# Kernel tuning notes

Hardware: AMD Instinct MI355X
Metric: run time of the kernel (lower is better)

Reference implementation:

```python
import jax, jax.numpy as jnp
import numpy as np
import math

B, S, D_MODEL = 2, 2048, 1024
H = 16
DK = D_MODEL // H          # 64, down-proj per-stream dim
NOPE, ROPE = 128, 64
D_HEAD = NOPE + ROPE       # 192 = d_latent // H
D_LATENT = H * D_HEAD      # 3072
ROT_DIM = 2 * ((ROPE // 2) // 2)  # rotary dim actually rotated = qk_rope_dim//2 = 32
EPS = 1e-6


def _rmsnorm(x, w):
    out = x * jax.lax.rsqrt(jnp.mean(x * x, axis=-1, keepdims=True) + EPS)
    return out * w


def _apply_rope(x):
    # x: [b, h, s, d]; rotate first ROT_DIM channels, interleaved pairing
    s = x.shape[-2]
    inv_freq = 1.0 / (10000.0 ** (jnp.arange(0, ROT_DIM, 2, dtype=jnp.float32) / ROT_DIM))
    freqs = jnp.arange(s, dtype=jnp.float32)[:, None] * inv_freq[None, :]  # [s, ROT_DIM//2]
    freqs = jnp.repeat(freqs, 2, axis=-1)  # [s, ROT_DIM], (f0,f0,f1,f1,...)
    cos, sin = jnp.cos(freqs), jnp.sin(freqs)
    xl, xr = x[..., :ROT_DIM], x[..., ROT_DIM:]
    x1, x2 = xl[..., 0::2], xl[..., 1::2]
    rot = jnp.stack([-x2, x1], axis=-1).reshape(xl.shape)
    xl = xl * cos + rot * sin
    return jnp.concatenate([xl, xr], axis=-1)


def setup_inputs() -> dict:
    key = jax.random.key(0)
    ks = jax.random.split(key, 5)
    sc = 0.02
    x = jax.random.normal(ks[0], (B, S, D_MODEL), jnp.float32)
    mask = jnp.broadcast_to(jnp.tril(jnp.ones((S, S), jnp.int32)), (B, S, S))
    w_down = jax.random.normal(ks[1], (D_MODEL, 3 * DK), jnp.float32) * sc
    rms_w = jnp.ones((3 * DK,), jnp.float32)
    w_up = jax.random.normal(ks[2], (3 * DK, 3 * D_LATENT), jnp.float32) * sc
    w_o = jax.random.normal(ks[3], (D_LATENT, D_MODEL), jnp.float32) * sc
    return {"x": x, "mask": mask, "w_down": w_down, "rms_w": rms_w, "w_up": w_up, "w_o": w_o}


def reference(x, mask, w_down, rms_w, w_up, w_o):
    h = x @ w_down                        # [b, s, 3*dk]
    h = _rmsnorm(h, rms_w)
    qkv = h @ w_up                        # [b, s, 3*d_latent]
    q, k, v = jnp.split(qkv, 3, axis=-1)  # each [b, s, d_latent]

    def to_heads(t):
        # einops '(d h)': d outer, h inner
        return t.reshape(B, S, D_HEAD, H).transpose(0, 3, 1, 2)  # [b, h, s, d]

    q, k, v = to_heads(q), to_heads(k), to_heads(v)
    q_nope, q_rope = q[..., :NOPE], q[..., NOPE:]
    k_nope, k_rope = k[..., :NOPE], k[..., NOPE:]
    q_rope = _apply_rope(q_rope)
    k_rope = _apply_rope(k_rope)

    scores = (jnp.einsum('bhid,bhjd->bhij', q_nope, k_nope)
              + jnp.einsum('bhid,bhjd->bhij', q_rope, k_rope))
    scores = scores / math.sqrt(NOPE + ROPE)
    scores = jnp.where(mask[:, None] == 0, -1e9, scores)
    attn = jax.nn.softmax(scores, axis=-1)

    out = jnp.einsum('bhij,bhjd->bhid', attn, v)        # [b, h, s, d]
    out = out.transpose(0, 2, 1, 3).reshape(B, S, D_LATENT)  # 'b h s d -> b s (h d)'
    return out @ w_o
```

## Files before the change

### kernel.cpp

```cpp
#include <hip/hip_runtime.h>
#include <stdint.h>
#include <stddef.h>


typedef __bf16 bf16x8 __attribute__((ext_vector_type(8)));
typedef float  f32x4  __attribute__((ext_vector_type(4)));

#define MFMA16x16(a,b,c) __builtin_amdgcn_mfma_f32_16x16x32_bf16((a),(b),(c),0,0,0)

__device__ __forceinline__ uint16_t f2bf(float f){
  union { float f; uint32_t u; } v; v.f = f;
  uint32_t u = v.u + 0x7fffu + ((v.u >> 16) & 1u);
  return (uint16_t)(u >> 16);
}
__device__ __forceinline__ bf16x8 load_frag(const uint16_t* p){
  uint4 u = *reinterpret_cast<const uint4*>(p);
  return __builtin_bit_cast(bf16x8, u);
}
__device__ __forceinline__ f32x4 fzero(){
  f32x4 z = {0.f, 0.f, 0.f, 0.f};
  return z;
}
__device__ __forceinline__ uint32_t pack2(float a, float b){
  return (uint32_t)f2bf(a) | ((uint32_t)f2bf(b) << 16);
}
__device__ __forceinline__ void gl2lds16(const uint16_t* g, uint16_t* l){
  __builtin_amdgcn_global_load_lds(
      (const __attribute__((address_space(1))) uint32_t*)g,
      (__attribute__((address_space(3))) uint32_t*)l,
      16, 0, 0);
}

__global__ __launch_bounds__(256) void k_transpose_cvt(const float* __restrict__ in,
                                                       uint16_t* __restrict__ out,
                                                       int R, int C){
  __shared__ float t[32][33];
  const int tc = blockIdx.x * 32;
  const int tr = blockIdx.y * 32;
  const int j = threadIdx.x & 31, i0 = threadIdx.x >> 5;
  for(int ii = 0; ii < 4; ++ii){
    int r = i0 + ii * 8;
    t[r][j] = in[(size_t)(tr + r) * C + tc + j];
  }
  __syncthreads();
  for(int ii = 0; ii < 4; ++ii){
    int c = i0 + ii * 8;
    out[(size_t)(tc + c) * R + tr + j] = f2bf(t[j][c]);
  }
}

__global__ __launch_bounds__(256) void k_down_mfma(const float* __restrict__ x,
                                                   const uint16_t* __restrict__ wdt,
                                                   const float* __restrict__ rms_w,
                                                   uint16_t* __restrict__ h_out){
  __shared__ __align__(16) uint16_t as[32 * 64];
  __shared__ float hsq[32];
  const int tid  = threadIdx.x;
  const int wave = tid >> 6, lane = tid & 63;
  const int ml = lane & 15, qd = lane >> 4;
  const int m0 = blockIdx.x * 32;
  const int n0w = wave * 48;
  if(tid < 32) hsq[tid] = 0.f;

  f32x4 acc[2][3];
#pragma unroll
  for(int mt = 0; mt < 2; ++mt)
#pragma unroll
    for(int nt = 0; nt < 3; ++nt) acc[mt][nt] = fzero();

  const int srow = tid >> 3, sc = tid & 7;
  for(int kt = 0; kt < 16; ++kt){
    const float* src = x + (size_t)(m0 + srow) * 1024 + kt * 64 + sc * 8;
    float4 a = *reinterpret_cast<const float4*>(src);
    float4 b = *reinterpret_cast<const float4*>(src + 4);
    uint4 pk;
    pk.x = pack2(a.x, a.y); pk.y = pack2(a.z, a.w);
    pk.z = pack2(b.x, b.y); pk.w = pack2(b.z, b.w);
    __syncthreads();
    *reinterpret_cast<uint4*>(as + srow * 64 + ((sc ^ (srow & 7)) * 8)) = pk;
    __syncthreads();
#pragma unroll
    for(int kk = 0; kk < 2; ++kk){
      bf16x8 af[2];
#pragma unroll
      for(int mt = 0; mt < 2; ++mt){
        int row = mt * 16 + ml;
        af[mt] = load_frag(as + row * 64 + (((kk * 4 + qd) ^ (row & 7)) * 8));
      }
#pragma unroll
      for(int nt = 0; nt < 3; ++nt){
        bf16x8 bfr = load_frag(wdt + (size_t)(n0w + nt * 16 + ml) * 1024 + kt * 64 + kk * 32 + qd * 8);
#pragma unroll
        for(int mt = 0; mt < 2; ++mt)
          acc[mt][nt] = MFMA16x16(af[mt], bfr, acc[mt][nt]);
      }
    }
  }
  __syncthreads();
#pragma unroll
  for(int mt = 0; mt < 2; ++mt)
#pragma unroll
    for(int r = 0; r < 4; ++r){
      float s = acc[mt][0][r]*acc[mt][0][r] + acc[mt][1][r]*acc[mt][1][r] + acc[mt][2][r]*acc[mt][2][r];
#pragma unroll
      for(int off = 1; off < 16; off <<= 1) s += __shfl_xor(s, off);
      if(ml == 0) atomicAdd(&hsq[mt * 16 + qd * 4 + r], s);
    }
  __syncthreads();
  float rw[3];
#pragma unroll
  for(int nt = 0; nt < 3; ++nt) rw[nt] = rms_w[n0w + nt * 16 + ml];
#pragma unroll
  for(int mt = 0; mt < 2; ++mt)
#pragma unroll
    for(int r = 0; r < 4; ++r){
      int row = mt * 16 + qd * 4 + r;
      float scl = rsqrtf(hsq[row] * (1.0f / 192.0f) + 1e-6f);
#pragma unroll
      for(int nt = 0; nt < 3; ++nt)
        h_out[(size_t)(m0 + row) * 192 + n0w + nt * 16 + ml] = f2bf(acc[mt][nt][r] * scl * rw[nt]);
    }
}

__global__ __launch_bounds__(256) void k_gemm_up(const uint16_t* __restrict__ hmat,
                                                 const uint16_t* __restrict__ wt,
                                                 uint16_t* __restrict__ q_t,
                                                 uint16_t* __restrict__ k_t,
                                                 uint16_t* __restrict__ v_t){
  __shared__ __align__(16) uint16_t rp[16 * 129 * 8];
  const int wave = threadIdx.x >> 6, lane = threadIdx.x & 63;
  const int ml = lane & 15, qd = lane >> 4;
  const int m0 = blockIdx.y * 32;
  const int bx = blockIdx.x;
  const int which = bx / 6;
  const int d0b = (bx % 6) * 32;
  const int n0w = bx * 512 + wave * 128;
  const int d0w = d0b + wave * 8;

  bf16x8 af[2][6];
#pragma unroll
  for(int mt = 0; mt < 2; ++mt)
#pragma unroll
    for(int kk = 0; kk < 6; ++kk)
      af[mt][kk] = load_frag(hmat + (size_t)(m0 + mt * 16 + ml) * 192 + kk * 32 + qd * 8);

  f32x4 acc[8][2];
#pragma unroll
  for(int nt = 0; nt < 8; ++nt){ acc[nt][0] = fzero(); acc[nt][1] = fzero(); }
#pragma unroll
  for(int nt = 0; nt < 8; ++nt){
#pragma unroll
    for(int kk = 0; kk < 6; ++kk){
      bf16x8 b = load_frag(wt + (size_t)(n0w + nt * 16 + ml) * 192 + kk * 32 + qd * 8);
      acc[nt][0] = MFMA16x16(af[0][kk], b, acc[nt][0]);
      acc[nt][1] = MFMA16x16(af[1][kk], b, acc[nt][1]);
    }
  }

  const int b   = m0 >> 11;
  const int s0  = m0 & 2047;
  const int kt2 = s0 >> 6;
  const int row0 = s0 & 63;
  uint4* rp4 = (uint4*)rp;

  if(which < 2){
    const float qs = which ? 1.0f : 0.07216878364870322f;
    const bool rope = (d0w >= 128) && (d0w < 160);
#pragma unroll
    for(int mt = 0; mt < 2; ++mt)
#pragma unroll
      for(int r = 0; r < 4; ++r){
        int t = mt * 16 + qd * 4 + r;
        int s = s0 + t;
        float v[8];
#pragma unroll
        for(int nt = 0; nt < 8; ++nt) v[nt] = acc[nt][mt][r] * qs;
        if(rope){
#pragma unroll
          for(int pi = 0; pi < 4; ++pi){
            int fi = (d0w + 2 * pi - 128) >> 1;
            float invf = __expf(-(float)fi * 0.5756462732485114f);
            float sn, cs;
            sincosf((float)s * invf, &sn, &cs);
            float e = v[2 * pi], o = v[2 * pi + 1];
            v[2 * pi]     = e * cs - o * sn;
            v[2 * pi + 1] = o * cs + e * sn;
          }
        }
        uint4 pk;
        pk.x = pack2(v[0], v[1]); pk.y = pack2(v[2], v[3]);
        pk.z = pack2(v[4], v[5]); pk.w = pack2(v[6], v[7]);
        rp4[ml * 129 + t * 4 + (wave ^ (t & 3))] = pk;
      }
  } else {
#pragma unroll
    for(int nt = 0; nt < 8; ++nt){
      int dl = wave * 8 + nt;
#pragma unroll
      for(int mt = 0; mt < 2; ++mt){
        int jc = mt * 2 + (qd >> 1);
        int slot = ml * 129 + dl * 4 + (jc ^ (dl & 3));
        uint2 pk;
        pk.x = pack2(acc[nt][mt][0], acc[nt][mt][1]);
        pk.y = pack2(acc[nt][mt][2], acc[nt][mt][3]);
        *(reinterpret_cast<uint2*>(rp + slot * 8) + (qd & 1)) = pk;
      }
    }
  }
  __syncthreads();

  if(which < 2){
    uint16_t* dst = which ? k_t : q_t;
    const int cb = d0b >> 3;
#pragma unroll
    for(int it = 0; it < 8; ++it){
      int h = wave * 4 + (it & 3), rhalf = it >> 2;
      int tloc = rhalf * 16 + (lane >> 2), p = lane & 3;
      int row = row0 + tloc;
      uint4 val = rp4[h * 129 + tloc * 4 + p];
      size_t off = ((size_t)(b * 16 + h) * 32 + kt2) * 12288
                 + (size_t)row * 192 + ((cb ^ (tloc & 4)) + p) * 8;
      *reinterpret_cast<uint4*>(dst + off) = val;
    }
  } else {
    const int cs0 = row0 >> 3;
#pragma unroll
    for(int it = 0; it < 8; ++it){
      int h = wave * 4 + (it & 3), dhalf = it >> 2;
      int dl = dhalf * 16 + (lane >> 2), p = lane & 3;
      uint4 val = rp4[h * 129 + dl * 4 + p];
      size_t off = ((size_t)(b * 16 + h) * 32 + kt2) * 12288
                 + (size_t)(d0b + dl) * 64 + ((cs0 ^ (dl & 4)) + p) * 8;
      *reinterpret_cast<uint4*>(v_t + off) = val;
    }
  }
}

__global__ __launch_bounds__(512, 2) void k_attn(const uint16_t* __restrict__ q_t,
                                                 const uint16_t* __restrict__ k_t,
                                                 const uint16_t* __restrict__ v_t,
                                                 uint16_t* __restrict__ attn_out){
  __shared__ __align__(16) uint16_t smem[61440];
  const int tid  = threadIdx.x;
  const int wave = tid >> 6;
  const int lane = tid & 63;
  const int ml   = lane & 15;
  const int qd   = lane >> 4;
  const int hw   = wave & 3;
  const int half = wave >> 2;
  const int bx   = blockIdx.x;
  const int bh   = bx & 31;
  const int s    = 15 - (bx >> 5);
  const int Lh   = 2 * s + 2;

  uint16_t* const psw = smem + 51200 + wave * 1280;

  const uint16_t* kbase = k_t + (size_t)bh * 393216;
  const uint16_t* vbase = v_t + (size_t)bh * 393216;
  const int hh = bh & 15, bb = bh >> 4;

  const int c_  = (lane & 3) ^ ((lane >> 3) & 3);
  const int s7_ = (lane >> 2) & 7;
  const int vg_ = (lane >> 2) * 64;
  const int voff0 = vg_ + ((c_ ^ s7_) * 8);
  const int voff1 = vg_ + (((4 + c_) ^ s7_) * 8);
  const int vpo = ml * 32 + ((qd ^ ((ml >> 1) & 3)) * 8);

  bf16x8 qf[2][6];
  {
    const uint16_t* qtb = q_t + ((size_t)bh * 32 + 2 * s + (hw >> 1)) * 12288;
#pragma unroll
    for(int t = 0; t < 2; ++t){
      int row = (hw & 1) * 32 + t * 16 + ml;
      const uint16_t* qr = qtb + (size_t)row * 192;
      int sw = row & 7;
#pragma unroll
      for(int kk = 0; kk < 6; ++kk)
        qf[t][kk] = load_frag(qr + (((kk * 4 + qd) ^ sw) * 8));
    }
  }

  {
    uint32_t* o01 = (uint32_t*)(smem + 24576 + (tid >> 8) * 6656 + 6144);
    uint32_t* o23 = (uint32_t*)(smem + 24576 + (2 + (tid >> 8)) * 6656 + 6144);
    o01[tid & 255] = 0x3F803F80u;
    o23[tid & 255] = 0x3F803F80u;
  }
  asm volatile("s_waitcnt lgkmcnt(0)" ::: "memory");

  auto stageKV = [&](int kt, int sel){
    const int b4 = half * 2 + sel;
#pragma unroll
    for(int it = 0; it < 3; ++it){
      int seg = hw * 3 + it;
      const uint16_t* ksrc = kbase + (size_t)(kt >> 1) * 12288 + (kt & 1) * 6144
                           + seg * 512 + lane * 8;
      gl2lds16(ksrc, smem + b4 * 6144 + seg * 512);
    }
    const int vo = (kt & 1) ? voff1 : voff0;
#pragma unroll
    for(int it = 0; it < 3; ++it){
      int seg = hw * 3 + it;
      const uint16_t* vsrc = vbase + (size_t)(kt >> 1) * 12288 + (size_t)seg * 1024 + vo;
      gl2lds16(vsrc, smem + 24576 + b4 * 6656 + seg * 512);
    }
  };

  const int kt0 = half * Lh;
  stageKV(kt0, 0);

  f32x4 o[2][13];
#pragma unroll
  for(int t = 0; t < 2; ++t)
#pragma unroll
    for(int i = 0; i < 13; ++i) o[t][i] = fzero();

  const int r0 = s * 128 + hw * 32;
  const int r1 = r0 + 16;
  int cur = 0;
  for(int i = 0; i < Lh; ++i){
    if(i + 1 < Lh){
      stageKV(kt0 + i + 1, cur ^ 1);
      __builtin_amdgcn_sched_barrier(0);
      asm volatile("s_waitcnt vmcnt(6)" ::: "memory");
      __builtin_amdgcn_sched_barrier(0);
    } else {
      asm volatile("s_waitcnt vmcnt(0)" ::: "memory");
      __builtin_amdgcn_sched_barrier(0);
    }
    __builtin_amdgcn_s_barrier();

    const int kl = (kt0 + i) * 32;
    if(kl <= r1 + 15){
      const uint16_t* kc = smem + (half * 2 + cur) * 6144;
      const uint16_t* vc = smem + 24576 + (half * 2 + cur) * 6656;
      const bool a0 = (kl <= r0 + 15);

      f32x4 sv[2][2];
      sv[0][0] = fzero(); sv[0][1] = fzero(); sv[1][0] = fzero(); sv[1][1] = fzero();
      __builtin_amdgcn_s_setprio(1);
#pragma unroll
      for(int nt = 0; nt < 2; ++nt){
        int row = nt * 16 + ml;
#pragma unroll
        for(int kk = 0; kk < 6; ++kk){
          bf16x8 bfr = load_frag(kc + row * 192 + (((kk * 4 + qd) ^ (row & 7)) * 8));
          if(a0) sv[0][nt] = MFMA16x16(qf[0][kk], bfr, sv[0][nt]);
          sv[1][nt] = MFMA16x16(qf[1][kk], bfr, sv[1][nt]);
        }
      }
      __builtin_amdgcn_s_setprio(0);

#pragma unroll
      for(int t = 0; t < 2; ++t){
        if(t == 0 && !a0) continue;
        const int rq = r0 + t * 16;
        const bool diag = (kl + 31 > rq);
#pragma unroll
        for(int nt = 0; nt < 2; ++nt)
#pragma unroll
          for(int r = 0; r < 4; ++r){
            float v = sv[t][nt][r];
            if(diag){
              int i2 = rq + qd * 4 + r;
              int j = kl + nt * 16 + ml;
              if(j > i2) v = -1e9f;
            }
            psw[(t * 16 + qd * 4 + r) * 40 + nt * 16 + ml] = f2bf(__expf(v));
          }
      }
      bf16x8 pa0 = load_frag(psw + ml * 40 + qd * 8);
      bf16x8 pa1 = load_frag(psw + (16 + ml) * 40 + qd * 8);
      __builtin_amdgcn_s_setprio(1);
#pragma unroll
      for(int dt = 0; dt < 13; ++dt){
        bf16x8 vbf = load_frag(vc + dt * 512 + vpo);
        if(a0) o[0][dt] = MFMA16x16(pa0, vbf, o[0][dt]);
        o[1][dt] = MFMA16x16(pa1, vbf, o[1][dt]);
      }
      __builtin_amdgcn_s_setprio(0);
    }
    __builtin_amdgcn_s_barrier();
    cur ^= 1;
  }

  f32x4* red = (f32x4*)smem;
  if(half == 1){
#pragma unroll
    for(int t = 0; t < 2; ++t)
#pragma unroll
      for(int dt = 0; dt < 13; ++dt)
        red[(hw * 2 + t) * 832 + lane * 13 + dt] = o[t][dt];
  }
  __syncthreads();
  if(half == 0){
#pragma unroll
    for(int t = 0; t < 2; ++t){
#pragma unroll
      for(int dt = 0; dt < 13; ++dt)
        o[t][dt] += red[(hw * 2 + t) * 832 + lane * 13 + dt];
      const int rq = r0 + t * 16;
#pragma unroll
      for(int r = 0; r < 4; ++r){
        int i2 = rq + qd * 4 + r;
        float inv = 1.0f / o[t][12][r];
        size_t obase = ((size_t)bb * 2048 + i2) * 3072 + hh * 192;
#pragma unroll
        for(int dt = 0; dt < 12; ++dt)
          attn_out[obase + dt * 16 + ml] = f2bf(o[t][dt][r] * inv);
      }
    }
  }
}

__global__ __launch_bounds__(256) void k_gemm_o_tile(const uint16_t* __restrict__ a,
                                                     const uint16_t* __restrict__ wt,
                                                     float* __restrict__ part){
  __shared__ __align__(16) uint16_t as[128 * 64];
  __shared__ __align__(16) uint16_t bs[128 * 64];
  const int wave = threadIdx.x >> 6, lane = threadIdx.x & 63;
  const int ml = lane & 15, qd = lane >> 4;
  const int m0 = blockIdx.y * 128, n0 = blockIdx.x * 128;
  const int kz = blockIdx.z;
  const int mo = (wave >> 1) * 64, no = (wave & 1) * 64;

  const int lrow = lane >> 3;
  const int gch  = (lane & 7) ^ (lrow & 7);
  const uint16_t* abase = a  + (size_t)(m0 + lrow) * 3072 + kz * 1536 + gch * 8;
  const uint16_t* bbase = wt + (size_t)(n0 + lrow) * 3072 + kz * 1536 + gch * 8;

  f32x4 acc[4][4];
#pragma unroll
  for(int mt = 0; mt < 4; ++mt)
#pragma unroll
    for(int nt = 0; nt < 4; ++nt) acc[mt][nt] = fzero();

  for(int kt = 0; kt < 24; ++kt){
    __syncthreads();
#pragma unroll
    for(int it = 0; it < 4; ++it){
      int seg = it * 4 + wave;
      gl2lds16(abase + (size_t)seg * 24576 + kt * 64, as + seg * 512);
      gl2lds16(bbase + (size_t)seg * 24576 + kt * 64, bs + seg * 512);
    }
    __syncthreads();
#pragma unroll
    for(int ks2 = 0; ks2 < 2; ++ks2){
      bf16x8 af[4], bfr[4];
#pragma unroll
      for(int mt = 0; mt < 4; ++mt){
        int row = mo + mt * 16 + ml;
        af[mt] = load_frag(as + row * 64 + (((ks2 * 4 + qd) ^ (row & 7)) * 8));
      }
#pragma unroll
      for(int nt = 0; nt < 4; ++nt){
        int row = no + nt * 16 + ml;
        bfr[nt] = load_frag(bs + row * 64 + (((ks2 * 4 + qd) ^ (row & 7)) * 8));
      }
#pragma unroll
      for(int mt = 0; mt < 4; ++mt)
#pragma unroll
        for(int nt = 0; nt < 4; ++nt)
          acc[mt][nt] = MFMA16x16(af[mt], bfr[nt], acc[mt][nt]);
    }
  }

  float* dst = part + (size_t)kz * 4096 * 1024;
#pragma unroll
  for(int mt = 0; mt < 4; ++mt)
#pragma unroll
    for(int nt = 0; nt < 4; ++nt)
#pragma unroll
      for(int r = 0; r < 4; ++r){
        int row = m0 + mo + mt * 16 + qd * 4 + r;
        int col = n0 + no + nt * 16 + ml;
        dst[(size_t)row * 1024 + col] = acc[mt][nt][r];
      }
}

__global__ __launch_bounds__(256) void k_addout(const float* __restrict__ part,
                                                float* __restrict__ out){
  int i = blockIdx.x * 256 + threadIdx.x;
  const float4* p0 = (const float4*)part;
  const float4* p1 = p0 + (size_t)1048576;
  float4 a = p0[i], b = p1[i];
  float4 c; c.x = a.x + b.x; c.y = a.y + b.y; c.z = a.z + b.z; c.w = a.w + b.w;
  ((float4*)out)[i] = c;
}


extern "C" void kernel_launch(void* const* d_in, const int* in_sizes, int n_in,
                              void* d_out, int out_size, void* d_ws, size_t ws_size,
                              hipStream_t stream) {
  (void)in_sizes; (void)n_in; (void)out_size; (void)ws_size;
  const float* x      = (const float*)d_in[0];
  const float* w_down = (const float*)d_in[2];
  const float* rms_w  = (const float*)d_in[3];
  const float* w_up   = (const float*)d_in[4];
  const float* w_o    = (const float*)d_in[5];
  float* out = (float*)d_out;

  char* ws = (char*)d_ws;
  uint16_t* h_bf   = (uint16_t*)(ws);
  uint16_t* w_up_t = (uint16_t*)(ws + 1572864);
  uint16_t* w_o_t  = (uint16_t*)(ws + 5111808);
  uint16_t* w_dn_t = (uint16_t*)(ws + 11403264);
  uint16_t* q_tb   = (uint16_t*)(ws + 11796480);
  uint16_t* k_tb   = (uint16_t*)(ws + 36962304);
  uint16_t* v_tb   = (uint16_t*)(ws + 62128128);
  uint16_t* attnO  = (uint16_t*)(ws + 87293952);
  float*    part   = (float*)(ws + 11796480);

  k_transpose_cvt<<<dim3(288, 6), 256, 0, stream>>>(w_up, w_up_t, 192, 9216);
  k_transpose_cvt<<<dim3(32, 96), 256, 0, stream>>>(w_o,  w_o_t,  3072, 1024);
  k_transpose_cvt<<<dim3(6, 32),  256, 0, stream>>>(w_down, w_dn_t, 1024, 192);
  k_down_mfma<<<128, 256, 0, stream>>>(x, w_dn_t, rms_w, h_bf);
  k_gemm_up<<<dim3(18, 128), 256, 0, stream>>>(h_bf, w_up_t, q_tb, k_tb, v_tb);
  k_attn<<<512, 512, 0, stream>>>(q_tb, k_tb, v_tb, attnO);
  k_gemm_o_tile<<<dim3(8, 32, 2), 256, 0, stream>>>(attnO, w_o_t, part);
  k_addout<<<4096, 256, 0, stream>>>(part, out);
}
```

Measured before the change: 342.9 us.

## Split attention work across 16 waves with one 16-row query tile each

```diff
diff --git a/kernel.cpp b/kernel.cpp
--- a/kernel.cpp
+++ b/kernel.cpp
@@ -236,24 +236,24 @@
   }
 }
 
-__global__ __launch_bounds__(512, 2) void k_attn(const uint16_t* __restrict__ q_t,
-                                                 const uint16_t* __restrict__ k_t,
-                                                 const uint16_t* __restrict__ v_t,
-                                                 uint16_t* __restrict__ attn_out){
+__global__ __launch_bounds__(1024, 1) void k_attn(const uint16_t* __restrict__ q_t,
+                                                  const uint16_t* __restrict__ k_t,
+                                                  const uint16_t* __restrict__ v_t,
+                                                  uint16_t* __restrict__ attn_out){
   __shared__ __align__(16) uint16_t smem[61440];
   const int tid  = threadIdx.x;
   const int wave = tid >> 6;
   const int lane = tid & 63;
   const int ml   = lane & 15;
   const int qd   = lane >> 4;
-  const int hw   = wave & 3;
-  const int half = wave >> 2;
+  const int hw   = wave & 7;
+  const int half = wave >> 3;
   const int bx   = blockIdx.x;
   const int bh   = bx & 31;
   const int s    = 15 - (bx >> 5);
   const int Lh   = 2 * s + 2;
 
-  uint16_t* const psw = smem + 51200 + wave * 1280;
+  uint16_t* const psw = smem + 51200 + wave * 640;
 
   const uint16_t* kbase = k_t + (size_t)bh * 393216;
   const uint16_t* vbase = v_t + (size_t)bh * 393216;
@@ -266,63 +266,52 @@
   const int voff1 = vg_ + (((4 + c_) ^ s7_) * 8);
   const int vpo = ml * 32 + ((qd ^ ((ml >> 1) & 3)) * 8);
 
-  bf16x8 qf[2][6];
+  bf16x8 qf[6];
   {
-    const uint16_t* qtb = q_t + ((size_t)bh * 32 + 2 * s + (hw >> 1)) * 12288;
-#pragma unroll
-    for(int t = 0; t < 2; ++t){
-      int row = (hw & 1) * 32 + t * 16 + ml;
-      const uint16_t* qr = qtb + (size_t)row * 192;
-      int sw = row & 7;
-#pragma unroll
-      for(int kk = 0; kk < 6; ++kk)
-        qf[t][kk] = load_frag(qr + (((kk * 4 + qd) ^ sw) * 8));
-    }
-  }
-
-  {
-    uint32_t* o01 = (uint32_t*)(smem + 24576 + (tid >> 8) * 6656 + 6144);
-    uint32_t* o23 = (uint32_t*)(smem + 24576 + (2 + (tid >> 8)) * 6656 + 6144);
-    o01[tid & 255] = 0x3F803F80u;
-    o23[tid & 255] = 0x3F803F80u;
-  }
+    const uint16_t* qtb = q_t + ((size_t)bh * 32 + 2 * s + (hw >> 2)) * 12288;
+    int row = (hw & 3) * 16 + ml;
+    const uint16_t* qr = qtb + (size_t)row * 192;
+    int sw = row & 7;
+#pragma unroll
+    for(int kk = 0; kk < 6; ++kk)
+      qf[kk] = load_frag(qr + (((kk * 4 + qd) ^ sw) * 8));
+  }
+
+  ((uint32_t*)(smem + 24576 + (tid >> 8) * 6656 + 6144))[tid & 255] = 0x3F803F80u;
   asm volatile("s_waitcnt lgkmcnt(0)" ::: "memory");
 
   auto stageKV = [&](int kt, int sel){
     const int b4 = half * 2 + sel;
+    const int vo = (kt & 1) ? voff1 : voff0;
 #pragma unroll
     for(int it = 0; it < 3; ++it){
       int seg = hw * 3 + it;
-      const uint16_t* ksrc = kbase + (size_t)(kt >> 1) * 12288 + (kt & 1) * 6144
-                           + seg * 512 + lane * 8;
-      gl2lds16(ksrc, smem + b4 * 6144 + seg * 512);
-    }
-    const int vo = (kt & 1) ? voff1 : voff0;
-#pragma unroll
-    for(int it = 0; it < 3; ++it){
-      int seg = hw * 3 + it;
-      const uint16_t* vsrc = vbase + (size_t)(kt >> 1) * 12288 + (size_t)seg * 1024 + vo;
-      gl2lds16(vsrc, smem + 24576 + b4 * 6656 + seg * 512);
+      if(seg < 12){
+        const uint16_t* ksrc = kbase + (size_t)(kt >> 1) * 12288 + (kt & 1) * 6144
+                             + seg * 512 + lane * 8;
+        gl2lds16(ksrc, smem + b4 * 6144 + seg * 512);
+      } else {
+        int vs = seg - 12;
+        const uint16_t* vsrc = vbase + (size_t)(kt >> 1) * 12288 + (size_t)vs * 1024 + vo;
+        gl2lds16(vsrc, smem + 24576 + b4 * 6656 + vs * 512);
+      }
     }
   };
 
   const int kt0 = half * Lh;
   stageKV(kt0, 0);
 
-  f32x4 o[2][13];
-#pragma unroll
-  for(int t = 0; t < 2; ++t)
-#pragma unroll
-    for(int i = 0; i < 13; ++i) o[t][i] = fzero();
-
-  const int r0 = s * 128 + hw * 32;
-  const int r1 = r0 + 16;
+  f32x4 o[13];
+#pragma unroll
+  for(int i = 0; i < 13; ++i) o[i] = fzero();
+
+  const int r0 = s * 128 + hw * 16;
   int cur = 0;
   for(int i = 0; i < Lh; ++i){
     if(i + 1 < Lh){
       stageKV(kt0 + i + 1, cur ^ 1);
       __builtin_amdgcn_sched_barrier(0);
-      asm volatile("s_waitcnt vmcnt(6)" ::: "memory");
+      asm volatile("s_waitcnt vmcnt(3)" ::: "memory");
       __builtin_amdgcn_sched_barrier(0);
     } else {
       asm volatile("s_waitcnt vmcnt(0)" ::: "memory");
@@ -331,52 +320,45 @@
     __builtin_amdgcn_s_barrier();
 
     const int kl = (kt0 + i) * 32;
-    if(kl <= r1 + 15){
+    if(kl <= r0 + 15){
       const uint16_t* kc = smem + (half * 2 + cur) * 6144;
       const uint16_t* vc = smem + 24576 + (half * 2 + cur) * 6656;
-      const bool a0 = (kl <= r0 + 15);
-
-      f32x4 sv[2][2];
-      sv[0][0] = fzero(); sv[0][1] = fzero(); sv[1][0] = fzero(); sv[1][1] = fzero();
+
+      float pp[2][4];
       __builtin_amdgcn_s_setprio(1);
 #pragma unroll
       for(int nt = 0; nt < 2; ++nt){
+        f32x4 a = fzero();
         int row = nt * 16 + ml;
 #pragma unroll
         for(int kk = 0; kk < 6; ++kk){
           bf16x8 bfr = load_frag(kc + row * 192 + (((kk * 4 + qd) ^ (row & 7)) * 8));
-          if(a0) sv[0][nt] = MFMA16x16(qf[0][kk], bfr, sv[0][nt]);
-          sv[1][nt] = MFMA16x16(qf[1][kk], bfr, sv[1][nt]);
+          a = MFMA16x16(qf[kk], bfr, a);
         }
+#pragma unroll
+        for(int r = 0; r < 4; ++r) pp[nt][r] = a[r];
       }
       __builtin_amdgcn_s_setprio(0);
 
-#pragma unroll
-      for(int t = 0; t < 2; ++t){
-        if(t == 0 && !a0) continue;
-        const int rq = r0 + t * 16;
-        const bool diag = (kl + 31 > rq);
-#pragma unroll
-        for(int nt = 0; nt < 2; ++nt)
-#pragma unroll
-          for(int r = 0; r < 4; ++r){
-            float v = sv[t][nt][r];
-            if(diag){
-              int i2 = rq + qd * 4 + r;
-              int j = kl + nt * 16 + ml;
-              if(j > i2) v = -1e9f;
-            }
-            psw[(t * 16 + qd * 4 + r) * 40 + nt * 16 + ml] = f2bf(__expf(v));
+      const bool diag = (kl + 31 > r0);
+#pragma unroll
+      for(int nt = 0; nt < 2; ++nt)
+#pragma unroll
+        for(int r = 0; r < 4; ++r){
+          float v = pp[nt][r];
+          if(diag){
+            int i2 = r0 + qd * 4 + r;
+            int j = kl + nt * 16 + ml;
+            if(j > i2) v = -1e9f;
           }
-      }
-      bf16x8 pa0 = load_frag(psw + ml * 40 + qd * 8);
-      bf16x8 pa1 = load_frag(psw + (16 + ml) * 40 + qd * 8);
+          psw[(qd * 4 + r) * 40 + nt * 16 + ml] = f2bf(__expf(v));
+        }
+      bf16x8 pa = load_frag(psw + ml * 40 + qd * 8);
       __builtin_amdgcn_s_setprio(1);
 #pragma unroll
       for(int dt = 0; dt < 13; ++dt){
         bf16x8 vbf = load_frag(vc + dt * 512 + vpo);
-        if(a0) o[0][dt] = MFMA16x16(pa0, vbf, o[0][dt]);
-        o[1][dt] = MFMA16x16(pa1, vbf, o[1][dt]);
+        o[dt] = MFMA16x16(pa, vbf, o[dt]);
       }
       __builtin_amdgcn_s_setprio(0);
     }
@@ -387,28 +369,22 @@
   f32x4* red = (f32x4*)smem;
   if(half == 1){
 #pragma unroll
-    for(int t = 0; t < 2; ++t)
-#pragma unroll
-      for(int dt = 0; dt < 13; ++dt)
-        red[(hw * 2 + t) * 832 + lane * 13 + dt] = o[t][dt];
+    for(int dt = 0; dt < 13; ++dt)
+      red[(hw * 64 + lane) * 13 + dt] = o[dt];
   }
   __syncthreads();
   if(half == 0){
 #pragma unroll
-    for(int t = 0; t < 2; ++t){
-#pragma unroll
-      for(int dt = 0; dt < 13; ++dt)
-        o[t][dt] += red[(hw * 2 + t) * 832 + lane * 13 + dt];
-      const int rq = r0 + t * 16;
-#pragma unroll
-      for(int r = 0; r < 4; ++r){
-        int i2 = rq + qd * 4 + r;
-        float inv = 1.0f / o[t][12][r];
-        size_t obase = ((size_t)bb * 2048 + i2) * 3072 + hh * 192;
-#pragma unroll
-        for(int dt = 0; dt < 12; ++dt)
-          attn_out[obase + dt * 16 + ml] = f2bf(o[t][dt][r] * inv);
-      }
+    for(int dt = 0; dt < 13; ++dt)
+      o[dt] += red[(hw * 64 + lane) * 13 + dt];
+#pragma unroll
+    for(int r = 0; r < 4; ++r){
+      int i2 = r0 + qd * 4 + r;
+      float inv = 1.0f / o[12][r];
+      size_t obase = ((size_t)bb * 2048 + i2) * 3072 + hh * 192;
+#pragma unroll
+      for(int dt = 0; dt < 12; ++dt)
+        attn_out[obase + dt * 16 + ml] = f2bf(o[dt][r] * inv);
     }
   }
 }
@@ -516,7 +492,7 @@
   k_transpose_cvt<<<dim3(6, 32),  256, 0, stream>>>(w_down, w_dn_t, 1024, 192);
   k_down_mfma<<<128, 256, 0, stream>>>(x, w_dn_t, rms_w, h_bf);
   k_gemm_up<<<dim3(18, 128), 256, 0, stream>>>(h_bf, w_up_t, q_tb, k_tb, v_tb);
-  k_attn<<<512, 512, 0, stream>>>(q_tb, k_tb, v_tb, attnO);
+  k_attn<<<512, 1024, 0, stream>>>(q_tb, k_tb, v_tb, attnO);
   k_gemm_o_tile<<<dim3(8, 32, 2), 256, 0, stream>>>(attnO, w_o_t, part);
   k_addout<<<4096, 256, 0, stream>>>(part, out);
 }
```

Result: no change. 336.3 us (-1.9%).

## Split attention PV over 16 waves and drop split-K output GEMM

Applied to the files above, without the earlier changes.

```diff
diff --git a/kernel.cpp b/kernel.cpp
--- a/kernel.cpp
+++ b/kernel.cpp
@@ -236,24 +236,26 @@
   }
 }
 
-__global__ __launch_bounds__(512, 2) void k_attn(const uint16_t* __restrict__ q_t,
-                                                 const uint16_t* __restrict__ k_t,
-                                                 const uint16_t* __restrict__ v_t,
-                                                 uint16_t* __restrict__ attn_out){
-  __shared__ __align__(16) uint16_t smem[61440];
+__global__ __launch_bounds__(1024, 1) void k_attn(const uint16_t* __restrict__ q_t,
+                                                  const uint16_t* __restrict__ k_t,
+                                                  const uint16_t* __restrict__ v_t,
+                                                  uint16_t* __restrict__ attn_out){
+  __shared__ __align__(16) uint16_t smem[59392];
   const int tid  = threadIdx.x;
   const int wave = tid >> 6;
   const int lane = tid & 63;
   const int ml   = lane & 15;
   const int qd   = lane >> 4;
-  const int hw   = wave & 3;
-  const int half = wave >> 2;
+  const int g    = wave & 3;
+  const int e    = (wave >> 2) & 1;
+  const int half = wave >> 3;
+  const int sseg = wave & 7;
   const int bx   = blockIdx.x;
   const int bh   = bx & 31;
   const int s    = 15 - (bx >> 5);
   const int Lh   = 2 * s + 2;
 
-  uint16_t* const psw = smem + 51200 + wave * 1280;
+  uint16_t* const psw = smem + 49152 + (g * 2 + half) * 1280;
 
   const uint16_t* kbase = k_t + (size_t)bh * 393216;
   const uint16_t* vbase = v_t + (size_t)bh * 393216;
@@ -266,63 +268,59 @@
   const int voff1 = vg_ + (((4 + c_) ^ s7_) * 8);
   const int vpo = ml * 32 + ((qd ^ ((ml >> 1) & 3)) * 8);
 
+  const uint4 onesu = {0x3F803F80u, 0x3F803F80u, 0x3F803F80u, 0x3F803F80u};
+  const bf16x8 vones = __builtin_bit_cast(bf16x8, onesu);
+
+  const int r0 = s * 128 + g * 32;
+
   bf16x8 qf[2][6];
-  {
-    const uint16_t* qtb = q_t + ((size_t)bh * 32 + 2 * s + (hw >> 1)) * 12288;
+  if(e == 0){
 #pragma unroll
     for(int t = 0; t < 2; ++t){
-      int row = (hw & 1) * 32 + t * 16 + ml;
-      const uint16_t* qr = qtb + (size_t)row * 192;
-      int sw = row & 7;
+      int rr = g * 32 + t * 16;
+      int rloc = (rr & 63) + ml;
+      const uint16_t* qtb = q_t + ((size_t)bh * 32 + 2 * s + (rr >> 6)) * 12288
+                          + (size_t)rloc * 192;
+      int sw = rloc & 7;
 #pragma unroll
       for(int kk = 0; kk < 6; ++kk)
-        qf[t][kk] = load_frag(qr + (((kk * 4 + qd) ^ sw) * 8));
-    }
-  }
-
-  {
-    uint32_t* o01 = (uint32_t*)(smem + 24576 + (tid >> 8) * 6656 + 6144);
-    uint32_t* o23 = (uint32_t*)(smem + 24576 + (2 + (tid >> 8)) * 6656 + 6144);
-    o01[tid & 255] = 0x3F803F80u;
-    o23[tid & 255] = 0x3F803F80u;
-  }
-  asm volatile("s_waitcnt lgkmcnt(0)" ::: "memory");
+        qf[t][kk] = load_frag(qtb + (((kk * 4 + qd) ^ sw) * 8));
+    }
+  }
 
   auto stageKV = [&](int kt, int sel){
     const int b4 = half * 2 + sel;
+    const int vo = (kt & 1) ? voff1 : voff0;
 #pragma unroll
     for(int it = 0; it < 3; ++it){
-      int seg = hw * 3 + it;
-      const uint16_t* ksrc = kbase + (size_t)(kt >> 1) * 12288 + (kt & 1) * 6144
-                           + seg * 512 + lane * 8;
-      gl2lds16(ksrc, smem + b4 * 6144 + seg * 512);
-    }
-    const int vo = (kt & 1) ? voff1 : voff0;
-#pragma unroll
-    for(int it = 0; it < 3; ++it){
-      int seg = hw * 3 + it;
-      const uint16_t* vsrc = vbase + (size_t)(kt >> 1) * 12288 + (size_t)seg * 1024 + vo;
-      gl2lds16(vsrc, smem + 24576 + b4 * 6656 + seg * 512);
+      int seg = sseg * 3 + it;
+      if(seg < 12){
+        const uint16_t* ksrc = kbase + (size_t)(kt >> 1) * 12288 + (kt & 1) * 6144
+                             + seg * 512 + lane * 8;
+        gl2lds16(ksrc, smem + b4 * 6144 + seg * 512);
+      } else {
+        int vs = seg - 12;
+        const uint16_t* vsrc = vbase + (size_t)(kt >> 1) * 12288 + (size_t)vs * 1024 + vo;
+        gl2lds16(vsrc, smem + 24576 + b4 * 6144 + vs * 512);
+      }
     }
   };
 
   const int kt0 = half * Lh;
   stageKV(kt0, 0);
 
-  f32x4 o[2][13];
+  f32x4 o[2][7];
 #pragma unroll
   for(int t = 0; t < 2; ++t)
 #pragma unroll
-    for(int i = 0; i < 13; ++i) o[t][i] = fzero();
-
-  const int r0 = s * 128 + hw * 32;
-  const int r1 = r0 + 16;
+    for(int i = 0; i < 7; ++i) o[t][i] = fzero();
+
   int cur = 0;
   for(int i = 0; i < Lh; ++i){
     if(i + 1 < Lh){
       stageKV(kt0 + i + 1, cur ^ 1);
       __builtin_amdgcn_sched_barrier(0);
-      asm volatile("s_waitcnt vmcnt(6)" ::: "memory");
+      asm volatile("s_waitcnt vmcnt(3)" ::: "memory");
       __builtin_amdgcn_sched_barrier(0);
     } else {
       asm volatile("s_waitcnt vmcnt(0)" ::: "memory");
@@ -331,11 +329,11 @@
     __builtin_amdgcn_s_barrier();
 
     const int kl = (kt0 + i) * 32;
-    if(kl <= r1 + 15){
+    const bool active = (kl <= r0 + 31);
+    const bool a0 = (kl <= r0 + 15);
+
+    if(active && e == 0){
       const uint16_t* kc = smem + (half * 2 + cur) * 6144;
-      const uint16_t* vc = smem + 24576 + (half * 2 + cur) * 6656;
-      const bool a0 = (kl <= r0 + 15);
-
       f32x4 sv[2][2];
       sv[0][0] = fzero(); sv[0][1] = fzero(); sv[1][0] = fzero(); sv[1][1] = fzero();
       __builtin_amdgcn_s_setprio(1);
@@ -350,7 +348,6 @@
         }
       }
       __builtin_amdgcn_s_setprio(0);
-
 #pragma unroll
       for(int t = 0; t < 2; ++t){
         if(t == 0 && !a0) continue;
@@ -368,15 +365,32 @@
             }
             psw[(t * 16 + qd * 4 + r) * 40 + nt * 16 + ml] = f2bf(__expf(v));
           }
-      }
+      asm volatile("s_waitcnt lgkmcnt(0)" ::: "memory");
+      }
+    }
+    __builtin_amdgcn_s_barrier();
+
+    if(active){
+      const uint16_t* vc = smem + 24576 + (half * 2 + cur) * 6144;
       bf16x8 pa0 = load_frag(psw + ml * 40 + qd * 8);
       bf16x8 pa1 = load_frag(psw + (16 + ml) * 40 + qd * 8);
       __builtin_amdgcn_s_setprio(1);
-#pragma unroll
-      for(int dt = 0; dt < 13; ++dt){
-        bf16x8 vbf = load_frag(vc + dt * 512 + vpo);
-        if(a0) o[0][dt] = MFMA16x16(pa0, vbf, o[0][dt]);
-        o[1][dt] = MFMA16x16(pa1, vbf, o[1][dt]);
+      if(e == 0){
+#pragma unroll
+        for(int d2 = 0; d2 < 6; ++d2){
+          bf16x8 vbf = load_frag(vc + d2 * 512 + vpo);
+          if(a0) o[0][d2] = MFMA16x16(pa0, vbf, o[0][d2]);
+          o[1][d2] = MFMA16x16(pa1, vbf, o[1][d2]);
+        }
+      } else {
+#pragma unroll
+        for(int d2 = 0; d2 < 6; ++d2){
+          bf16x8 vbf = load_frag(vc + (6 + d2) * 512 + vpo);
+          if(a0) o[0][d2] = MFMA16x16(pa0, vbf, o[0][d2]);
+          o[1][d2] = MFMA16x16(pa1, vbf, o[1][d2]);
+        }
+        if(a0) o[0][6] = MFMA16x16(pa0, vones, o[0][6]);
+        o[1][6] = MFMA16x16(pa1, vones, o[1][6]);
       }
       __builtin_amdgcn_s_setprio(0);
     }
@@ -384,30 +398,45 @@
     cur ^= 1;
   }
 
+  __syncthreads();
   f32x4* red = (f32x4*)smem;
+  float* dnf = (float*)(((char*)smem) + 114688);
+  const int rbase = (g * 2 + e) * 896;
   if(half == 1){
 #pragma unroll
     for(int t = 0; t < 2; ++t)
 #pragma unroll
-      for(int dt = 0; dt < 13; ++dt)
-        red[(hw * 2 + t) * 832 + lane * 13 + dt] = o[t][dt];
+      for(int d2 = 0; d2 < 7; ++d2)
+        red[rbase + (t * 7 + d2) * 64 + lane] = o[t][d2];
   }
   __syncthreads();
   if(half == 0){
 #pragma unroll
+    for(int t = 0; t < 2; ++t)
+#pragma unroll
+      for(int d2 = 0; d2 < 7; ++d2)
+        o[t][d2] += red[rbase + (t * 7 + d2) * 64 + lane];
+    if(e == 1 && ml == 0){
+#pragma unroll
+      for(int t = 0; t < 2; ++t)
+#pragma unroll
+        for(int r = 0; r < 4; ++r)
+          dnf[g * 32 + t * 16 + qd * 4 + r] = o[t][6][r];
+    }
+  }
+  __syncthreads();
+  if(half == 0){
+#pragma unroll
     for(int t = 0; t < 2; ++t){
-#pragma unroll
-      for(int dt = 0; dt < 13; ++dt)
-        o[t][dt] += red[(hw * 2 + t) * 832 + lane * 13 + dt];
       const int rq = r0 + t * 16;
 #pragma unroll
       for(int r = 0; r < 4; ++r){
         int i2 = rq + qd * 4 + r;
-        float inv = 1.0f / o[t][12][r];
+        float inv = 1.0f / dnf[g * 32 + t * 16 + qd * 4 + r];
         size_t obase = ((size_t)bb * 2048 + i2) * 3072 + hh * 192;
 #pragma unroll
-        for(int dt = 0; dt < 12; ++dt)
-          attn_out[obase + dt * 16 + ml] = f2bf(o[t][dt][r] * inv);
+        for(int d2 = 0; d2 < 6; ++d2)
+          attn_out[obase + (e * 6 + d2) * 16 + ml] = f2bf(o[t][d2][r] * inv);
       }
     }
   }
@@ -415,19 +444,18 @@
 
 __global__ __launch_bounds__(256) void k_gemm_o_tile(const uint16_t* __restrict__ a,
                                                      const uint16_t* __restrict__ wt,
-                                                     float* __restrict__ part){
+                                                     float* __restrict__ out){
   __shared__ __align__(16) uint16_t as[128 * 64];
   __shared__ __align__(16) uint16_t bs[128 * 64];
   const int wave = threadIdx.x >> 6, lane = threadIdx.x & 63;
   const int ml = lane & 15, qd = lane >> 4;
   const int m0 = blockIdx.y * 128, n0 = blockIdx.x * 128;
-  const int kz = blockIdx.z;
   const int mo = (wave >> 1) * 64, no = (wave & 1) * 64;
 
   const int lrow = lane >> 3;
   const int gch  = (lane & 7) ^ (lrow & 7);
-  const uint16_t* abase = a  + (size_t)(m0 + lrow) * 3072 + kz * 1536 + gch * 8;
-  const uint16_t* bbase = wt + (size_t)(n0 + lrow) * 3072 + kz * 1536 + gch * 8;
+  const uint16_t* abase = a  + (size_t)(m0 + lrow) * 3072 + gch * 8;
+  const uint16_t* bbase = wt + (size_t)(n0 + lrow) * 3072 + gch * 8;
 
   f32x4 acc[4][4];
 #pragma unroll
@@ -435,7 +463,7 @@
 #pragma unroll
     for(int nt = 0; nt < 4; ++nt) acc[mt][nt] = fzero();
 
-  for(int kt = 0; kt < 24; ++kt){
+  for(int kt = 0; kt < 48; ++kt){
     __syncthreads();
 #pragma unroll
     for(int it = 0; it < 4; ++it){
@@ -465,7 +493,6 @@
     }
   }
 
-  float* dst = part + (size_t)kz * 4096 * 1024;
 #pragma unroll
   for(int mt = 0; mt < 4; ++mt)
 #pragma unroll
@@ -474,18 +501,8 @@
       for(int r = 0; r < 4; ++r){
         int row = m0 + mo + mt * 16 + qd * 4 + r;
         int col = n0 + no + nt * 16 + ml;
-        dst[(size_t)row * 1024 + col] = acc[mt][nt][r];
-      }
-}
-
-__global__ __launch_bounds__(256) void k_addout(const float* __restrict__ part,
-                                                float* __restrict__ out){
-  int i = blockIdx.x * 256 + threadIdx.x;
-  const float4* p0 = (const float4*)part;
-  const float4* p1 = p0 + (size_t)1048576;
-  float4 a = p0[i], b = p1[i];
-  float4 c; c.x = a.x + b.x; c.y = a.y + b.y; c.z = a.z + b.z; c.w = a.w + b.w;
-  ((float4*)out)[i] = c;
+        out[(size_t)row * 1024 + col] = acc[mt][nt][r];
+      }
 }
 
 
@@ -509,14 +526,12 @@
   uint16_t* k_tb   = (uint16_t*)(ws + 36962304);
   uint16_t* v_tb   = (uint16_t*)(ws + 62128128);
   uint16_t* attnO  = (uint16_t*)(ws + 87293952);
-  float*    part   = (float*)(ws + 11796480);
 
   k_transpose_cvt<<<dim3(288, 6), 256, 0, stream>>>(w_up, w_up_t, 192, 9216);
   k_transpose_cvt<<<dim3(32, 96), 256, 0, stream>>>(w_o,  w_o_t,  3072, 1024);
   k_transpose_cvt<<<dim3(6, 32),  256, 0, stream>>>(w_down, w_dn_t, 1024, 192);
   k_down_mfma<<<128, 256, 0, stream>>>(x, w_dn_t, rms_w, h_bf);
   k_gemm_up<<<dim3(18, 128), 256, 0, stream>>>(h_bf, w_up_t, q_tb, k_tb, v_tb);
-  k_attn<<<512, 512, 0, stream>>>(q_tb, k_tb, v_tb, attnO);
-  k_gemm_o_tile<<<dim3(8, 32, 2), 256, 0, stream>>>(attnO, w_o_t, part);
-  k_addout<<<4096, 256, 0, stream>>>(part, out);
-}
+  k_attn<<<512, 1024, 0, stream>>>(q_tb, k_tb, v_tb, attnO);
+  k_gemm_o_tile<<<dim3(8, 32), 256, 0, stream>>>(attnO, w_o_t, out);
+}
```

Result: slower. 577.4 us (+68.4%).
